# Kernel optimization log

Measured on AMD Instinct MI355X. Metric: run time of the kernel, lower is better.

Reference implementation:

```python
import jax, jax.numpy as jnp
import numpy as np

T = S = 1024
B = 8
HID = 1024
H = 16
D = HID // H          # head_size = 64
RELK = 16             # max relative position (clip window)
NEG = -1e9


def setup_inputs() -> dict:
    key = jax.random.key(0)
    ks = jax.random.split(key, 12)
    inv = 1.0 / np.sqrt(HID)
    inp = {
        'q': jax.random.normal(ks[0], (T, B, HID), jnp.float32),
        'k': jax.random.normal(ks[1], (S, B, HID), jnp.float32),
        'v': jax.random.normal(ks[2], (S, B, HID), jnp.float32),
        # additive float mask (B,T,S): causal, masked positions = -1e9
        'mask': jnp.broadcast_to(jnp.triu(jnp.full((T, S), NEG, jnp.float32), k=1), (B, T, S)),
        'Wq': jax.random.normal(ks[3], (HID, HID), jnp.float32) * inv,
        'bq': jnp.zeros((HID,), jnp.float32),
        'Wk': jax.random.normal(ks[4], (HID, HID), jnp.float32) * inv,
        'bk': jnp.zeros((HID,), jnp.float32),
        'Wv': jax.random.normal(ks[5], (HID, HID), jnp.float32) * inv,
        'bv': jnp.zeros((HID,), jnp.float32),
        'Wo': jax.random.normal(ks[6], (HID, HID), jnp.float32) * inv,
        'bo': jnp.zeros((HID,), jnp.float32),
        'rel_k_table': jax.random.normal(ks[7], (2 * RELK + 1, D), jnp.float32) * 0.02,
        'rel_v_table': jax.random.normal(ks[8], (2 * RELK + 1, D), jnp.float32) * 0.02,
    }
    return inp


def _rel_index(t, s):
    # clipped relative position index (t, s) -> [0, 2*RELK]
    return jnp.clip(jnp.arange(s)[None, :] - jnp.arange(t)[:, None], -RELK, RELK) + RELK


def reference(q, k, v, mask, Wq, bq, Wk, bk, Wv, bv, Wo, bo, rel_k_table, rel_v_table):
    t, b, _ = q.shape
    scaling = D ** -0.5
    # projections; torch Linear: x @ W^T + b, here weights stored (in,out)
    qh = ((q @ Wq + bq) * scaling).reshape(t, b * H, D).transpose(1, 0, 2)  # (BH,T,D)
    kh = (k @ Wk + bk).reshape(-1, b * H, D).transpose(1, 0, 2)            # (BH,S,D)
    vh = (v @ Wv + bv).reshape(-1, b * H, D).transpose(1, 0, 2)            # (BH,S,D)
    s = kh.shape[1]

    score = jnp.einsum('ntd,nsd->nts', qh, kh)                 # (BH,T,S)
    idx = _rel_index(t, s)
    rel_k = rel_k_table[idx]                                   # (T,S,D)
    score = score + jnp.einsum('ntd,tsd->nts', qh, rel_k)      # relative-pos bias on scores

    score = (score.reshape(b, H, t, s) + mask[:, None]).reshape(b * H, t, s)
    attn = jax.nn.softmax(score, axis=-1)                      # dropout=0 (eval)

    o = jnp.einsum('nts,nsd->ntd', attn, vh)                   # (BH,T,D)
    rel_v = rel_v_table[idx]                                   # (T,S,D)
    o = o + jnp.einsum('nts,tsd->ntd', attn, rel_v)            # relative-pos bias on values

    o = o.transpose(1, 0, 2).reshape(t, b, H * D)              # (T,B,hidden)
    return o @ Wo + bo
```

## Files before the change

### kernel.cpp

```cpp
#include <hip/hip_runtime.h>

typedef unsigned short u16;
typedef __bf16 bf16x8 __attribute__((ext_vector_type(8)));
typedef __bf16 bf16x4v __attribute__((ext_vector_type(4)));
typedef short s16x4 __attribute__((ext_vector_type(4)));
typedef unsigned short u16x8 __attribute__((ext_vector_type(8)));
typedef unsigned short u16x4 __attribute__((ext_vector_type(4)));
typedef float f32x4 __attribute__((ext_vector_type(4)));


__device__ __forceinline__ u16 f2bf(float f) {
  union { float f; unsigned u; } v; v.f = f;
  unsigned r = v.u + 0x7fffu + ((v.u >> 16) & 1u);
  return (u16)(r >> 16);
}
__device__ __forceinline__ u16x8 pack_trunc8(float4 a, float4 b) {
  u16x8 t;
  t[0] = (u16)(__float_as_uint(a.x) >> 16); t[1] = (u16)(__float_as_uint(a.y) >> 16);
  t[2] = (u16)(__float_as_uint(a.z) >> 16); t[3] = (u16)(__float_as_uint(a.w) >> 16);
  t[4] = (u16)(__float_as_uint(b.x) >> 16); t[5] = (u16)(__float_as_uint(b.y) >> 16);
  t[6] = (u16)(__float_as_uint(b.z) >> 16); t[7] = (u16)(__float_as_uint(b.w) >> 16);
  return t;
}
__device__ __forceinline__ void barrier_lgkm() {
  __asm__ volatile("s_waitcnt lgkmcnt(0)\ns_barrier" ::: "memory");
}
typedef const __attribute__((address_space(1))) void* gas_ptr;
typedef __attribute__((address_space(3))) void* las_ptr;
__device__ __forceinline__ void load_lds16(const void* g, void* l) {
  __builtin_amdgcn_global_load_lds((gas_ptr)g, (las_ptr)l, 16, 0, 0);
}
__device__ __forceinline__ f32x4 mfma16(u16x4 a, u16x4 b, f32x4 c) {
#if __has_builtin(__builtin_amdgcn_mfma_f32_16x16x16_bf16)
  return __builtin_amdgcn_mfma_f32_16x16x16_bf16(
      __builtin_bit_cast(bf16x4v, a), __builtin_bit_cast(bf16x4v, b), c, 0, 0, 0);
#elif __has_builtin(__builtin_amdgcn_mfma_f32_16x16x16bf16_1k)
  return __builtin_amdgcn_mfma_f32_16x16x16bf16_1k(
      __builtin_bit_cast(s16x4, a), __builtin_bit_cast(s16x4, b), c, 0, 0, 0);
#else
  f32x4 d;
  __asm__ volatile("v_mfma_f32_16x16x16_bf16 %0, %1, %2, %3"
                   : "=v"(d) : "v"(a), "v"(b), "v"(c));
  return d;
#endif
}

__device__ __forceinline__ void transpose_body(const float* in, u16* out) {
  __shared__ u16 tile[64][65];
  const int r0 = blockIdx.y * 64, c0 = blockIdx.x * 64;
  const int tid = threadIdx.x;
  const int tr = tid >> 4, tc4 = (tid & 15) * 4;
#pragma unroll
  for (int p = 0; p < 4; ++p) {
    int r = tr + p * 16;
    float4 vv = *(const float4*)&in[(size_t)(r0 + r) * 1024 + c0 + tc4];
    tile[r][tc4 + 0] = f2bf(vv.x); tile[r][tc4 + 1] = f2bf(vv.y);
    tile[r][tc4 + 2] = f2bf(vv.z); tile[r][tc4 + 3] = f2bf(vv.w);
  }
  __syncthreads();
#pragma unroll
  for (int p = 0; p < 4; ++p) {
    int rr = tr + p * 16;
    ushort4 ov;
    ov.x = tile[tc4 + 0][rr]; ov.y = tile[tc4 + 1][rr];
    ov.z = tile[tc4 + 2][rr]; ov.w = tile[tc4 + 3][rr];
    *(ushort4*)&out[(size_t)(c0 + rr) * 1024 + r0 + tc4] = ov;
  }
}
__global__ __launch_bounds__(256) void transpose_cvt3_kernel(
    const float* w0, const float* w1, const float* w2,
    u16* o0, u16* o1, u16* o2)
{
  const float* in = blockIdx.z == 0 ? w0 : (blockIdx.z == 1 ? w1 : w2);
  u16* out = blockIdx.z == 0 ? o0 : (blockIdx.z == 1 ? o1 : o2);
  transpose_body(in, out);
}
__global__ __launch_bounds__(256) void transpose_cvt_kernel(
    const float* in, u16* out) { transpose_body(in, out); }

__global__ __launch_bounds__(256) void cvt2_kernel(
    const float* __restrict__ a, const float* __restrict__ b,
    u16* __restrict__ oa, u16* __restrict__ ob)
{
  const float* in = blockIdx.z ? b : a;
  u16* out = blockIdx.z ? ob : oa;
  const int n8 = (8192 * 1024) / 8;
  for (int i = blockIdx.x * 256 + threadIdx.x; i < n8; i += gridDim.x * 256) {
    float4 x = ((const float4*)in)[i * 2];
    float4 y = ((const float4*)in)[i * 2 + 1];
    *(u16x8*)&out[(size_t)i * 8] = pack_trunc8(x, y);
  }
}

struct GemmArgs {
  const u16* A; const u16* BT; const float* bias; void* out;
  float scale; int mode;
};

__global__ __launch_bounds__(256) void gemm_lds_kernel(GemmArgs g0, GemmArgs g1)
{
  __shared__ __align__(16) u16 smem[128 * 136];
  const GemmArgs g = blockIdx.z ? g1 : g0;
  const u16* __restrict__ A = g.A;
  const u16* __restrict__ BT = g.BT;
  const int tid = threadIdx.x;
  const int wave = tid >> 6, lane = tid & 63;
  const int quad = lane >> 4, l16 = lane & 15;
  const int wave_m = wave >> 1, wave_n = wave & 1;
  const int m0 = blockIdx.x * 128, n0 = blockIdx.y * 128;

  const int crow = tid >> 2;
  const int cq = (((tid & 3) ^ ((tid >> 3) & 3))) * 8;
  const int qswr = (quad ^ ((l16 >> 1) & 3)) * 8;

  f32x4 acc[4][4] = {};

  auto STAGE = [&](int bo, int kb) {
    const size_t ka = (size_t)kb * 32 + cq;
    load_lds16(&A [(size_t)(m0 + crow)      * 1024 + ka], &smem[bo + tid * 8]);
    load_lds16(&A [(size_t)(m0 + 64 + crow) * 1024 + ka], &smem[bo + 2048 + tid * 8]);
    load_lds16(&BT[(size_t)(n0 + crow)      * 1024 + ka], &smem[bo + 4096 + tid * 8]);
    load_lds16(&BT[(size_t)(n0 + 64 + crow) * 1024 + ka], &smem[bo + 6144 + tid * 8]);
  };

  STAGE(0, 0);
  __syncthreads();
  int cur = 0;
  for (int kb = 0; kb < 32; ++kb) {
    if (kb + 1 < 32) STAGE(cur ^ 8192, kb + 1);
    const u16* As = &smem[cur];
    const u16* Bs = &smem[cur + 4096];
    bf16x8 af[4], bfr[4];
#pragma unroll
    for (int mt = 0; mt < 4; ++mt)
      af[mt] = *(const bf16x8*)&As[(wave_m * 64 + mt * 16 + l16) * 32 + qswr];
#pragma unroll
    for (int nt = 0; nt < 4; ++nt)
      bfr[nt] = *(const bf16x8*)&Bs[(wave_n * 64 + nt * 16 + l16) * 32 + qswr];
#pragma unroll
    for (int mt = 0; mt < 4; ++mt)
#pragma unroll
      for (int nt = 0; nt < 4; ++nt)
        acc[mt][nt] = __builtin_amdgcn_mfma_f32_16x16x32_bf16(af[mt], bfr[nt], acc[mt][nt], 0, 0, 0);
    __syncthreads();
    cur ^= 8192;
  }

  const float scale = g.scale;
  if (g.mode == 0) {
#pragma unroll
    for (int mt = 0; mt < 4; ++mt)
#pragma unroll
      for (int nt = 0; nt < 4; ++nt) {
        int nn = n0 + wave_n * 64 + nt * 16 + l16;
        float bval = g.bias[nn];
#pragma unroll
        for (int reg = 0; reg < 4; ++reg) {
          int mm = m0 + wave_m * 64 + mt * 16 + quad * 4 + reg;
          ((float*)g.out)[(size_t)mm * 1024 + nn] = (acc[mt][nt][reg] + bval) * scale;
        }
      }
  } else {
    __syncthreads();
    u16* Cs = smem;
#pragma unroll
    for (int mt = 0; mt < 4; ++mt)
#pragma unroll
      for (int nt = 0; nt < 4; ++nt) {
        int nnl = wave_n * 64 + nt * 16 + l16;
        float bval = g.bias[n0 + nnl];
#pragma unroll
        for (int reg = 0; reg < 4; ++reg) {
          int mml = wave_m * 64 + mt * 16 + quad * 4 + reg;
          Cs[mml * 136 + nnl] = f2bf((acc[mt][nt][reg] + bval) * scale);
        }
      }
    __syncthreads();
    u16* out = (u16*)g.out;
    if (g.mode == 1) {
      int row = tid >> 1, half = tid & 1;
      int mm = m0 + row;
      int tt = mm >> 3, bbv = mm & 7;
      int hh = (n0 >> 6) + half;
      u16* dst = &out[(((size_t)(bbv * 16 + hh)) * 1024 + tt) * 64];
#pragma unroll
      for (int i = 0; i < 8; ++i)
        *(u16x8*)&dst[i * 8] = *(const u16x8*)&Cs[row * 136 + half * 64 + i * 8];
    } else {
      int t0 = m0 >> 3;
#pragma unroll
      for (int rr = 0; rr < 4; ++rr) {
        int rid = tid * 4 + rr;
        int nnv = rid >> 3, bbv = rid & 7;
        int hh = (n0 + nnv) >> 6, dd = (n0 + nnv) & 63;
        u16* dst = &out[(((size_t)(bbv * 16 + hh)) * 64 + dd) * 1024 + t0];
        u16x8 w0, w1;
#pragma unroll
        for (int t = 0; t < 8; ++t) w0[t] = Cs[(t * 8 + bbv) * 136 + nnv];
#pragma unroll
        for (int t = 0; t < 8; ++t) w1[t] = Cs[((t + 8) * 8 + bbv) * 136 + nnv];
        *(u16x8*)&dst[0] = w0;
        *(u16x8*)&dst[8] = w1;
      }
    }
  }
}

__global__ __launch_bounds__(256, 4) void attn_kernel(
    const u16* __restrict__ qh, const u16* __restrict__ kh,
    const u16* __restrict__ vt, const float* __restrict__ relk,
    const float* __restrict__ relv, u16* __restrict__ octx)
{
  const int n = blockIdx.x;
  const int q0 = (15 - blockIdx.y) * 64;
  const int tid = threadIdx.x;
  const int wave = tid >> 6, lane = tid & 63;
  const int quad = lane >> 4, l16 = lane & 15;
  const int rowi = wave * 16 + l16;
  const int trow = q0 + rowi;

  __shared__ __align__(16) u16 Ks[64 * 72];
  __shared__ __align__(16) u16 Vs[64 * 72];
  __shared__ float qrelS[64 * 17];
  __shared__ float wvS[17 * 64];
  __shared__ float relvS[17 * 64];

  const int diag = q0 >> 6;
  const int ntiles = diag + 1;

  bf16x8 qf[2];
#pragma unroll
  for (int kc = 0; kc < 2; ++kc)
    qf[kc] = *(const bf16x8*)&qh[((size_t)n * 1024 + trow) * 64 + kc * 32 + quad * 8];

  u16x8 kreg[2], vreg[2];
#pragma unroll
  for (int j = 0; j < 2; ++j) {
    int c = j * 256 + tid;
    kreg[j] = *(const u16x8*)&kh[((size_t)n * 1024 + (c >> 3)) * 64 + (c & 7) * 8];
    vreg[j] = *(const u16x8*)&vt[((size_t)n * 64 + (c >> 3)) * 1024 + (c & 7) * 8];
  }
  for (int i = tid; i < 17 * 64; i += 256) { wvS[i] = relk[i]; relvS[i] = relv[i]; }
  __syncthreads();

  float qreg[16];
#pragma unroll
  for (int kc = 0; kc < 2; ++kc)
#pragma unroll
    for (int jj = 0; jj < 8; ++jj)
      qreg[kc * 8 + jj] = (float)qf[kc][jj];
  float qrel0 = 0.f;
  for (int r = 0; r <= 16; ++r) {
    float s = 0.f;
#pragma unroll
    for (int kc = 0; kc < 2; ++kc)
#pragma unroll
      for (int jj = 0; jj < 8; ++jj)
        s += qreg[kc * 8 + jj] * wvS[r * 64 + kc * 32 + quad * 8 + jj];
    s += __shfl_xor(s, 16);
    s += __shfl_xor(s, 32);
    if (r == 0) qrel0 = s;
    if (quad == 0) qrelS[rowi * 17 + r] = s;
  }
  __syncthreads();
  for (int i = tid; i < 17 * 64; i += 256) wvS[i] = 0.f;
  __syncthreads();

  f32x4 oacc[4] = {};
  float lrow = 0.f;

  for (int st = 0; st < ntiles; ++st) {
    const int s0 = st * 64;
    if (st) barrier_lgkm();
#pragma unroll
    for (int j = 0; j < 2; ++j) {
      int c = j * 256 + tid;
      *(u16x8*)&Ks[(c >> 3) * 72 + (c & 7) * 8] = kreg[j];
      *(u16x8*)&Vs[(c >> 3) * 72 + (c & 7) * 8] = vreg[j];
    }
    barrier_lgkm();
    if (st + 1 < ntiles) {
      int s1 = s0 + 64;
#pragma unroll
      for (int j = 0; j < 2; ++j) {
        int c = j * 256 + tid;
        kreg[j] = *(const u16x8*)&kh[((size_t)n * 1024 + s1 + (c >> 3)) * 64 + (c & 7) * 8];
        vreg[j] = *(const u16x8*)&vt[((size_t)n * 64 + (c >> 3)) * 1024 + s1 + (c & 7) * 8];
      }
    }

    f32x4 sc[4];
#pragma unroll
    for (int j = 0; j < 4; ++j) {
      f32x4 c4 = {};
#pragma unroll
      for (int kc = 0; kc < 2; ++kc) {
        bf16x8 kf = *(const bf16x8*)&Ks[(j * 16 + l16) * 72 + kc * 32 + quad * 8];
        c4 = __builtin_amdgcn_mfma_f32_16x16x32_bf16(kf, qf[kc], c4, 0, 0, 0);
      }
      sc[j] = c4;
    }

    u16x4 pfrag[4];
    if (st < diag - 1) {
#pragma unroll
      for (int j = 0; j < 4; ++j) {
        u16x4 pk;
#pragma unroll
        for (int reg = 0; reg < 4; ++reg) {
          float pv = __expf(sc[j][reg] + qrel0 - 8.f);
          lrow += pv;
          pk[reg] = f2bf(pv);
        }
        pfrag[j] = pk;
      }
    } else {
#pragma unroll
      for (int j = 0; j < 4; ++j) {
        u16x4 pk;
#pragma unroll
        for (int reg = 0; reg < 4; ++reg) {
          int sel = s0 + j * 16 + quad * 4 + reg;
          int dt = trow - sel;
          float pv = 0.f;
          if (dt >= 0) {
            int r = (dt < 16) ? (16 - dt) : 0;
            pv = __expf(sc[j][reg] + qrelS[rowi * 17 + r] - 8.f);
            if (dt < 16) wvS[rowi * 17 + (16 - dt)] = pv;
          }
          lrow += pv;
          pk[reg] = f2bf(pv);
        }
        pfrag[j] = pk;
      }
    }

#pragma unroll
    for (int nt = 0; nt < 4; ++nt)
#pragma unroll
      for (int j = 0; j < 4; ++j) {
        u16x4 vfrag = *(const u16x4*)&Vs[(nt * 16 + l16) * 72 + j * 16 + quad * 4];
        oacc[nt] = mfma16(vfrag, pfrag[j], oacc[nt]);
      }
  }

  lrow += __shfl_xor(lrow, 16);
  lrow += __shfl_xor(lrow, 32);

  float wvr[17];
  float bsum = 0.f;
#pragma unroll
  for (int r = 1; r <= 16; ++r) { wvr[r] = wvS[rowi * 17 + r]; bsum += wvr[r]; }
  wvr[0] = lrow - bsum;
  float linv = 1.f / lrow;

  const int hh = n & 15, bb = n >> 4;
  size_t base = ((size_t)trow * 8 + bb) * 1024 + hh * 64;
#pragma unroll
  for (int nt = 0; nt < 4; ++nt) {
    u16x4 ov;
#pragma unroll
    for (int reg = 0; reg < 4; ++reg) {
      int d = nt * 16 + quad * 4 + reg;
      float rv = 0.f;
#pragma unroll
      for (int r = 0; r <= 16; ++r) rv += wvr[r] * relvS[r * 64 + d];
      ov[reg] = f2bf((oacc[nt][reg] + rv) * linv);
    }
    *(u16x4*)&octx[base + nt * 16 + quad * 4] = ov;
  }
}

extern "C" void kernel_launch(void* const* d_in, const int* in_sizes, int n_in,
                              void* d_out, int out_size, void* d_ws, size_t ws_size,
                              hipStream_t stream) {
  (void)in_sizes; (void)n_in; (void)out_size; (void)ws_size;
  const float* q    = (const float*)d_in[0];
  const float* k    = (const float*)d_in[1];
  const float* v    = (const float*)d_in[2];
  const float* Wq   = (const float*)d_in[4];
  const float* bq   = (const float*)d_in[5];
  const float* Wk   = (const float*)d_in[6];
  const float* bk   = (const float*)d_in[7];
  const float* Wv   = (const float*)d_in[8];
  const float* bv   = (const float*)d_in[9];
  const float* Wo   = (const float*)d_in[10];
  const float* bo   = (const float*)d_in[11];
  const float* relk = (const float*)d_in[12];
  const float* relv = (const float*)d_in[13];
  float* out = (float*)d_out;

  char* ws = (char*)d_ws;
  u16* vt   = (u16*)(ws);
  u16* qh   = (u16*)(ws + ((size_t)16 << 20));
  u16* kh   = (u16*)(ws + ((size_t)32 << 20));
  u16* octx = (u16*)(ws + ((size_t)48 << 20));
  u16* wqt  = (u16*)(ws + ((size_t)48 << 20));
  u16* wkt  = (u16*)(ws + ((size_t)50 << 20));
  u16* wvt  = (u16*)(ws + ((size_t)52 << 20));
  u16* wot  = kh;
  u16* qbf  = (u16*)d_out;
  u16* kbf  = (u16*)d_out + ((size_t)8 << 20);
  u16* vbf  = (u16*)d_out;

  dim3 blk(256);
  transpose_cvt3_kernel<<<dim3(16, 16, 3), blk, 0, stream>>>(Wq, Wk, Wv, wqt, wkt, wvt);

  cvt2_kernel<<<dim3(2048, 1, 2), blk, 0, stream>>>(q, k, qbf, kbf);
  GemmArgs gq{qbf, wqt, bq, qh, 0.125f, 1};
  GemmArgs gk{kbf, wkt, bk, kh, 1.0f,   1};
  gemm_lds_kernel<<<dim3(64, 8, 2), blk, 0, stream>>>(gq, gk);

  cvt2_kernel<<<dim3(2048, 1, 1), blk, 0, stream>>>(v, v, vbf, vbf);
  GemmArgs gv{vbf, wvt, bv, vt, 1.0f, 2};
  gemm_lds_kernel<<<dim3(64, 8, 1), blk, 0, stream>>>(gv, gv);

  attn_kernel<<<dim3(128, 16), blk, 0, stream>>>(qh, kh, vt, relk, relv, octx);

  transpose_cvt_kernel<<<dim3(16, 16), blk, 0, stream>>>(Wo, wot);

  GemmArgs go{octx, wot, bo, out, 1.0f, 0};
  gemm_lds_kernel<<<dim3(64, 8, 1), blk, 0, stream>>>(go, go);
}
```

Before: 358.9 us.

## Load K/V fragments directly from global memory, drop LDS staging and barriers

Result: slower. 499.0 us (+39.1%).

```diff
diff --git a/kernel.cpp b/kernel.cpp
--- a/kernel.cpp
+++ b/kernel.cpp
@@ -21,9 +21,6 @@
   t[4] = (u16)(__float_as_uint(b.x) >> 16); t[5] = (u16)(__float_as_uint(b.y) >> 16);
   t[6] = (u16)(__float_as_uint(b.z) >> 16); t[7] = (u16)(__float_as_uint(b.w) >> 16);
   return t;
-}
-__device__ __forceinline__ void barrier_lgkm() {
-  __asm__ volatile("s_waitcnt lgkmcnt(0)\ns_barrier" ::: "memory");
 }
 typedef const __attribute__((address_space(1))) void* gas_ptr;
 typedef __attribute__((address_space(3))) void* las_ptr;
@@ -219,8 +216,6 @@
   const int rowi = wave * 16 + l16;
   const int trow = q0 + rowi;
 
-  __shared__ __align__(16) u16 Ks[64 * 72];
-  __shared__ __align__(16) u16 Vs[64 * 72];
   __shared__ float qrelS[64 * 17];
   __shared__ float wvS[17 * 64];
   __shared__ float relvS[17 * 64];
@@ -233,13 +228,6 @@
   for (int kc = 0; kc < 2; ++kc)
     qf[kc] = *(const bf16x8*)&qh[((size_t)n * 1024 + trow) * 64 + kc * 32 + quad * 8];
 
-  u16x8 kreg[2], vreg[2];
-#pragma unroll
-  for (int j = 0; j < 2; ++j) {
-    int c = j * 256 + tid;
-    kreg[j] = *(const u16x8*)&kh[((size_t)n * 1024 + (c >> 3)) * 64 + (c & 7) * 8];
-    vreg[j] = *(const u16x8*)&vt[((size_t)n * 64 + (c >> 3)) * 1024 + (c & 7) * 8];
-  }
   for (int i = tid; i < 17 * 64; i += 256) { wvS[i] = relk[i]; relvS[i] = relv[i]; }
   __syncthreads();
 
@@ -269,37 +257,36 @@
   f32x4 oacc[4] = {};
   float lrow = 0.f;
 
+  const u16* __restrict__ khn = kh + (size_t)n * 1024 * 64;
+  const u16* __restrict__ vtn = vt + (size_t)n * 64 * 1024;
+
   for (int st = 0; st < ntiles; ++st) {
     const int s0 = st * 64;
-    if (st) barrier_lgkm();
-#pragma unroll
-    for (int j = 0; j < 2; ++j) {
-      int c = j * 256 + tid;
-      *(u16x8*)&Ks[(c >> 3) * 72 + (c & 7) * 8] = kreg[j];
-      *(u16x8*)&Vs[(c >> 3) * 72 + (c & 7) * 8] = vreg[j];
-    }
-    barrier_lgkm();
-    if (st + 1 < ntiles) {
-      int s1 = s0 + 64;
-#pragma unroll
-      for (int j = 0; j < 2; ++j) {
-        int c = j * 256 + tid;
-        kreg[j] = *(const u16x8*)&kh[((size_t)n * 1024 + s1 + (c >> 3)) * 64 + (c & 7) * 8];
-        vreg[j] = *(const u16x8*)&vt[((size_t)n * 64 + (c >> 3)) * 1024 + s1 + (c & 7) * 8];
-      }
-    }
+
+    bf16x8 kf[4][2];
+#pragma unroll
+    for (int j = 0; j < 4; ++j)
+#pragma unroll
+      for (int kc = 0; kc < 2; ++kc)
+        kf[j][kc] = *(const bf16x8*)&khn[(size_t)(s0 + j * 16 + l16) * 64 + kc * 32 + quad * 8];
 
     f32x4 sc[4];
+    __builtin_amdgcn_s_setprio(1);
 #pragma unroll
     for (int j = 0; j < 4; ++j) {
       f32x4 c4 = {};
-#pragma unroll
-      for (int kc = 0; kc < 2; ++kc) {
-        bf16x8 kf = *(const bf16x8*)&Ks[(j * 16 + l16) * 72 + kc * 32 + quad * 8];
-        c4 = __builtin_amdgcn_mfma_f32_16x16x32_bf16(kf, qf[kc], c4, 0, 0, 0);
-      }
+      c4 = __builtin_amdgcn_mfma_f32_16x16x32_bf16(kf[j][0], qf[0], c4, 0, 0, 0);
+      c4 = __builtin_amdgcn_mfma_f32_16x16x32_bf16(kf[j][1], qf[1], c4, 0, 0, 0);
       sc[j] = c4;
     }
+    __builtin_amdgcn_s_setprio(0);
+
+    u16x4 vf[4][4];
+#pragma unroll
+    for (int nt = 0; nt < 4; ++nt)
+#pragma unroll
+      for (int j = 0; j < 4; ++j)
+        vf[nt][j] = *(const u16x4*)&vtn[(size_t)(nt * 16 + l16) * 1024 + s0 + j * 16 + quad * 4];
 
     u16x4 pfrag[4];
     if (st < diag - 1) {
@@ -335,13 +322,13 @@
       }
     }
 
+    __builtin_amdgcn_s_setprio(1);
 #pragma unroll
     for (int nt = 0; nt < 4; ++nt)
 #pragma unroll
-      for (int j = 0; j < 4; ++j) {
-        u16x4 vfrag = *(const u16x4*)&Vs[(nt * 16 + l16) * 72 + j * 16 + quad * 4];
-        oacc[nt] = mfma16(vfrag, pfrag[j], oacc[nt]);
-      }
+      for (int j = 0; j < 4; ++j)
+        oacc[nt] = mfma16(vf[nt][j], pfrag[j], oacc[nt]);
+    __builtin_amdgcn_s_setprio(0);
   }
 
   lrow += __shfl_xor(lrow, 16);
```
